# Kernel tuning notes

Hardware: AMD Instinct MI355X
Metric: run time of the kernel (lower is better)

The kernel has to match this reference:

```python
import jax, jax.numpy as jnp
import numpy as np

T, HID, H, KV, D = 2048, 2048, 16, 8, 128
EPS = 1e-6
THETA = 10000.0


def setup_inputs() -> dict:
    key = jax.random.key(0)
    ks = jax.random.split(key, 4)
    return {
        "positions": jnp.arange(T, dtype=jnp.int32),
        "hidden_states": jax.random.normal(ks[0], (T, HID), dtype=jnp.float32),
        "layernorm_weight": jnp.ones((HID,), dtype=jnp.float32),
        "qkv_weight": jax.random.normal(ks[1], ((H + 2 * KV) * D, HID), dtype=jnp.float32) * 0.02,
        "q_norm_weight": jnp.ones((D,), dtype=jnp.float32),
        "k_norm_weight": jnp.ones((D,), dtype=jnp.float32),
        "o_weight": jax.random.normal(ks[2], (HID, H * D), dtype=jnp.float32) * 0.02,
    }


def _rms(x, w, eps=EPS):
    var = jnp.mean(jnp.square(x), axis=-1, keepdims=True)
    return x * jax.lax.rsqrt(var + eps) * w


def _rope(x, pos):
    # NeoX-style rotary over full head_dim. x: [T, nH, D]
    inv_freq = 1.0 / (THETA ** (jnp.arange(0, D, 2, dtype=jnp.float32) / D))
    ang = pos.astype(jnp.float32)[:, None] * inv_freq  # [T, D/2]
    cos, sin = jnp.cos(ang)[:, None, :], jnp.sin(ang)[:, None, :]
    x1, x2 = x[..., : D // 2], x[..., D // 2 :]
    return jnp.concatenate([x1 * cos - x2 * sin, x2 * cos + x1 * sin], axis=-1)


def reference(positions, hidden_states, layernorm_weight, qkv_weight,
              q_norm_weight, k_norm_weight, o_weight):
    # Fused RMSNorm + QKV projection
    normed = _rms(hidden_states, layernorm_weight)                 # [T, HID]
    qkv = normed @ qkv_weight.T                                    # [T, (H+2KV)*D]
    q, k, v = jnp.split(qkv, [H * D, (H + KV) * D], axis=-1)
    q = _rms(q.reshape(T, H, D), q_norm_weight)                    # per-head q norm
    k = _rms(k.reshape(T, KV, D), k_norm_weight)                   # per-head k norm
    v = v.reshape(T, KV, D)
    # RoPE
    q = _rope(q, positions)
    k = _rope(k, positions)
    # GQA causal attention
    scale = D ** -0.5
    kr = jnp.repeat(k, H // KV, axis=1)                            # [T, H, D]
    vr = jnp.repeat(v, H // KV, axis=1)
    scores = jnp.einsum("qhd,khd->hqk", q, kr) * scale             # [H, T, T]
    mask = jnp.tril(jnp.ones((T, T), dtype=bool))
    scores = jnp.where(mask[None], scores, jnp.finfo(scores.dtype).min)
    attn = jax.nn.softmax(scores, axis=-1)
    out = jnp.einsum("hqk,khd->qhd", attn, vr).reshape(T, H * D)
    return out @ o_weight.T                                        # [T, HID]
```

## Files before the change

kernel.cpp:

```cpp
#include <hip/hip_runtime.h>
#include <cstdint>
#include <cstddef>

typedef __bf16 bf16;
typedef __attribute__((ext_vector_type(8))) __bf16 bf16x8;
typedef __attribute__((ext_vector_type(4))) __bf16 bf16x4v;
typedef __attribute__((ext_vector_type(4))) float f32x4;
typedef __attribute__((ext_vector_type(4))) short short4v;

#define T_N   2048
#define HID_N 2048
#define NH    16
#define NKV   8
#define HD    128

#define MFMA(a, b, c) __builtin_amdgcn_mfma_f32_16x16x32_bf16((a), (b), (c), 0, 0, 0)

__device__ __forceinline__ f32x4 MFMA16(short4v a, short4v b, f32x4 c) {
#if __has_builtin(__builtin_amdgcn_mfma_f32_16x16x16bf16_1k)
    return __builtin_amdgcn_mfma_f32_16x16x16bf16_1k(a, b, c, 0, 0, 0);
#else
    asm volatile("v_mfma_f32_16x16x16_bf16 %0, %1, %2, %0\n\ts_nop 7\n\ts_nop 7"
                 : "+v"(c) : "v"(a), "v"(b));
    return c;
#endif
}

__device__ __forceinline__ void gl_lds16(const void* g, void* l) {
    __builtin_amdgcn_global_load_lds(
        (const __attribute__((address_space(1))) unsigned int*)g,
        (__attribute__((address_space(3))) unsigned int*)l,
        16, 0, 0);
}

__device__ __forceinline__ uint32_t pk2(float a, float b) {
    union { bf16 h; unsigned short u; } ca, cb;
    ca.h = (bf16)a; cb.h = (bf16)b;
    return ((uint32_t)cb.u << 16) | ca.u;
}

__global__ __launch_bounds__(256) void k_f2b(const float* __restrict__ in,
                                             bf16* __restrict__ out, int n) {
    int i = (blockIdx.x * 256 + threadIdx.x) * 8;
    if (i >= n) return;
    const float4* p = (const float4*)(in + i);
    float4 a = p[0], b = p[1];
    bf16x8 v;
    v[0] = (bf16)a.x; v[1] = (bf16)a.y; v[2] = (bf16)a.z; v[3] = (bf16)a.w;
    v[4] = (bf16)b.x; v[5] = (bf16)b.y; v[6] = (bf16)b.z; v[7] = (bf16)b.w;
    *(bf16x8*)(out + i) = v;
}

__global__ __launch_bounds__(256) void k_rmsnorm(const float* __restrict__ x,
                                                 const float* __restrict__ w,
                                                 bf16* __restrict__ out) {
    int row = blockIdx.x, tid = threadIdx.x;
    const float* xr = x + (size_t)row * HID_N;
    float4 a = ((const float4*)xr)[tid * 2];
    float4 b = ((const float4*)xr)[tid * 2 + 1];
    float ss = a.x*a.x + a.y*a.y + a.z*a.z + a.w*a.w
             + b.x*b.x + b.y*b.y + b.z*b.z + b.w*b.w;
    #pragma unroll
    for (int m = 32; m; m >>= 1) ss += __shfl_xor(ss, m);
    __shared__ float red[4];
    if ((tid & 63) == 0) red[tid >> 6] = ss;
    __syncthreads();
    float tot = red[0] + red[1] + red[2] + red[3];
    float rs = rsqrtf(tot * (1.0f / HID_N) + 1e-6f);
    const float4* wr = (const float4*)(w + tid * 8);
    float4 wa = wr[0], wb = wr[1];
    bf16x8 v;
    v[0] = (bf16)(a.x * rs * wa.x); v[1] = (bf16)(a.y * rs * wa.y);
    v[2] = (bf16)(a.z * rs * wa.z); v[3] = (bf16)(a.w * rs * wa.w);
    v[4] = (bf16)(b.x * rs * wb.x); v[5] = (bf16)(b.y * rs * wb.y);
    v[6] = (bf16)(b.z * rs * wb.z); v[7] = (bf16)(b.w * rs * wb.w);
    *(bf16x8*)(out + (size_t)row * HID_N + tid * 8) = v;
}

__global__ __launch_bounds__(256, 2) void k_gemm_bt(const bf16* __restrict__ A,
                                                    const bf16* __restrict__ B,
                                                    float* __restrict__ C,
                                                    int M, int N, int K) {
    __shared__ __attribute__((aligned(16))) bf16 As[128 * 64];
    __shared__ __attribute__((aligned(16))) bf16 Bs[128 * 64];
    const int tid = threadIdx.x;
    const int lane = tid & 63, wid = tid >> 6;
    const int wm = wid >> 1, wn = wid & 1;
    const int r = lane & 15, g = lane >> 4;
    const size_t bm = (size_t)blockIdx.y * 128, bn = (size_t)blockIdx.x * 128;

    f32x4 acc[4][4] = {};

    const int srow = tid >> 3;
    const int schk = tid & 7;

    for (int k0 = 0; k0 < K; k0 += 64) {
        __syncthreads();
        #pragma unroll
        for (int c = 0; c < 4; c++) {
            int row = c * 32 + srow;
            int ka = (schk ^ (row & 7)) << 3;
            gl_lds16(A + (bm + row) * (size_t)K + k0 + ka,
                     (char*)As + c * 4096 + tid * 16);
            gl_lds16(B + (bn + row) * (size_t)K + k0 + ka,
                     (char*)Bs + c * 4096 + tid * 16);
        }
        __syncthreads();
        #pragma unroll
        for (int kk = 0; kk < 2; kk++) {
            bf16x8 af[4], bfr[4];
            #pragma unroll
            for (int m = 0; m < 4; m++) {
                int row = wm * 64 + m * 16 + r;
                af[m] = *(const bf16x8*)(As + row * 64 + (((kk * 4 + g) ^ (row & 7)) << 3));
            }
            #pragma unroll
            for (int n = 0; n < 4; n++) {
                int row = wn * 64 + n * 16 + r;
                bfr[n] = *(const bf16x8*)(Bs + row * 64 + (((kk * 4 + g) ^ (row & 7)) << 3));
            }
            #pragma unroll
            for (int m = 0; m < 4; m++)
                #pragma unroll
                for (int n = 0; n < 4; n++)
                    acc[m][n] = MFMA(af[m], bfr[n], acc[m][n]);
        }
    }
    #pragma unroll
    for (int m = 0; m < 4; m++)
        #pragma unroll
        for (int n = 0; n < 4; n++)
            #pragma unroll
            for (int j = 0; j < 4; j++) {
                size_t row = bm + wm * 64 + m * 16 + g * 4 + j;
                size_t col = bn + wn * 64 + n * 16 + r;
                C[row * (size_t)N + col] = acc[m][n][j];
            }
}

__global__ __launch_bounds__(128) void k_normrope(const float* __restrict__ qkv,
                                                  const float* __restrict__ qw,
                                                  const float* __restrict__ kw,
                                                  const int* __restrict__ pos,
                                                  bf16* __restrict__ q,
                                                  bf16* __restrict__ k,
                                                  bf16* __restrict__ v) {
    int t = blockIdx.x, hs = blockIdx.y, d = threadIdx.x;
    const float* base = qkv + (size_t)t * 4096;
    if (hs >= 24) {
        int hv = hs - 24;
        v[((size_t)t * NKV + hv) * HD + d] = (bf16)base[3072 + hv * 128 + d];
        return;
    }
    bool isq = hs < 16;
    int h = isq ? hs : hs - 16;
    float x = isq ? base[h * 128 + d] : base[2048 + h * 128 + d];
    float ss = x * x;
    #pragma unroll
    for (int m = 32; m; m >>= 1) ss += __shfl_xor(ss, m);
    __shared__ float red[2];
    if ((d & 63) == 0) red[d >> 6] = ss;
    __syncthreads();
    float rs = rsqrtf((red[0] + red[1]) * (1.0f / HD) + 1e-6f);
    float nx = x * rs * (isq ? qw[d] : kw[d]);
    __shared__ float sh[128];
    sh[d] = nx;
    __syncthreads();
    float other = sh[d ^ 64];
    int j = d & 63;
    float ang = (float)pos[t] * __powf(10000.f, -(float)j * (1.f / 64.f));
    float s, c;
    __sincosf(ang, &s, &c);
    float o = (d < 64) ? (nx * c - other * s) : (nx * c + other * s);
    bf16* dst = isq ? (q + ((size_t)t * NH + h) * HD + d)
                    : (k + ((size_t)t * NKV + h) * HD + d);
    *dst = (bf16)o;
}

__global__ __launch_bounds__(256, 2) void k_flash(const bf16* __restrict__ Q,
                                                  const bf16* __restrict__ K,
                                                  const bf16* __restrict__ V,
                                                  bf16* __restrict__ O) {
    __shared__ __attribute__((aligned(16))) bf16 Ks2[2][64 * 128];
    __shared__ __attribute__((aligned(16))) bf16 Vt2[2][128 * 64];

    const int tid = threadIdx.x, lane = tid & 63, w = tid >> 6;
    const int r = lane & 15, g = lane >> 4;
    const int h = blockIdx.x, by = blockIdx.y;
    const int qt = (by < 16) ? (2 * by) : (63 - 2 * by);
    const int q0 = qt * 64;
    const int gh = h >> 1;
    const int q0w = q0 + w * 16;

    const int rowk = tid >> 4, posc = tid & 15;
    const int vd = tid & 127, vhalf = tid >> 7;

    bf16x8 qf[4];
    #pragma unroll
    for (int ks = 0; ks < 4; ks++)
        qf[ks] = *(const bf16x8*)(Q + ((size_t)(q0w + r) * NH + h) * HD + ks * 32 + g * 8);

    f32x4 acc[8] = {};
    float m_run = -1e30f, l_run = 0.f;
    const float scale = 0.08838834764831845f;
    const int nt = qt + 1;

    {
        #pragma unroll
        for (int c = 0; c < 4; c++) {
            int row = c * 16 + rowk;
            int srcc = posc ^ (row & 7);
            gl_lds16(K + ((size_t)row * NKV + gh) * HD + srcc * 8,
                     (char*)&Ks2[0][0] + c * 4096 + tid * 16);
        }
        bf16x8 vr[4];
        #pragma unroll
        for (int it = 0; it < 4; it++) {
            int kb = vhalf + it * 2;
            const bf16* src = V + ((size_t)(kb * 8) * NKV + gh) * HD + vd;
            #pragma unroll
            for (int i = 0; i < 8; i++) vr[it][i] = src[(size_t)i * (NKV * HD)];
        }
        #pragma unroll
        for (int it = 0; it < 4; it++) {
            int kb = vhalf + it * 2;
            *(bf16x8*)(&Vt2[0][0] + vd * 64 + ((kb ^ (vd & 7)) * 8)) = vr[it];
        }
        __syncthreads();
    }

    for (int t = 0; t < nt; ++t) {
        const int b = t & 1;
        const int kv0 = t * 64;
        const bool pf = (t + 1 < nt);
        bf16x8 vr[4];
        if (pf) {
            const int kv1 = kv0 + 64;
            #pragma unroll
            for (int c = 0; c < 4; c++) {
                int row = c * 16 + rowk;
                int srcc = posc ^ (row & 7);
                gl_lds16(K + ((size_t)(kv1 + row) * NKV + gh) * HD + srcc * 8,
                         (char*)&Ks2[0][0] + (b ^ 1) * 16384 + c * 4096 + tid * 16);
            }
            #pragma unroll
            for (int it = 0; it < 4; it++) {
                int kb = vhalf + it * 2;
                const bf16* src = V + ((size_t)(kv1 + kb * 8) * NKV + gh) * HD + vd;
                #pragma unroll
                for (int i = 0; i < 8; i++) vr[it][i] = src[(size_t)i * (NKV * HD)];
            }
        }
        {
            const bf16* Kb = &Ks2[b][0];
            const char* Vb = (const char*)&Vt2[b][0];
            float sc[4][4];
            __builtin_amdgcn_s_setprio(1);
            #pragma unroll
            for (int t4 = 0; t4 < 4; t4++) {
                f32x4 S = {};
                #pragma unroll
                for (int ks = 0; ks < 4; ks++) {
                    int row = t4 * 16 + r;
                    bf16x8 kf = *(const bf16x8*)(Kb + row * 128 + (((4 * ks + g) ^ (row & 7)) * 8));
                    S = MFMA(kf, qf[ks], S);
                }
                #pragma unroll
                for (int j = 0; j < 4; j++) {
                    int kg = kv0 + t4 * 16 + 4 * g + j;
                    sc[t4][j] = (kg <= q0w + r) ? S[j] * scale : -1e30f;
                }
            }
            __builtin_amdgcn_s_setprio(0);
            float mx = sc[0][0];
            #pragma unroll
            for (int t4 = 0; t4 < 4; t4++)
                #pragma unroll
                for (int j = 0; j < 4; j++) mx = fmaxf(mx, sc[t4][j]);
            mx = fmaxf(mx, __shfl_xor(mx, 16));
            mx = fmaxf(mx, __shfl_xor(mx, 32));
            float mn = fmaxf(m_run, mx);
            float alpha = __expf(m_run - mn);
            m_run = mn;
            float rsum = 0.f;
            #pragma unroll
            for (int t4 = 0; t4 < 4; t4++)
                #pragma unroll
                for (int j = 0; j < 4; j++) {
                    sc[t4][j] = __expf(sc[t4][j] - mn);
                    rsum += sc[t4][j];
                }
            rsum += __shfl_xor(rsum, 16);
            rsum += __shfl_xor(rsum, 32);
            l_run = l_run * alpha + rsum;
            #pragma unroll
            for (int f = 0; f < 8; f++)
                #pragma unroll
                for (int j = 0; j < 4; j++) acc[f][j] *= alpha;
            union PB { uint32_t u[2]; short4v s; };
            PB pbu[4];
            #pragma unroll
            for (int t4 = 0; t4 < 4; t4++) {
                pbu[t4].u[0] = pk2(sc[t4][0], sc[t4][1]);
                pbu[t4].u[1] = pk2(sc[t4][2], sc[t4][3]);
            }
            __builtin_amdgcn_s_setprio(1);
            #pragma unroll
            for (int f = 0; f < 8; f++) {
                #pragma unroll
                for (int t4 = 0; t4 < 4; t4++) {
                    short4v vf = *(const short4v*)(Vb + f * 2048 + r * 128 +
                                  (((2 * t4 + (g >> 1)) ^ (r & 7)) * 16) + (g & 1) * 8);
                    acc[f] = MFMA16(vf, pbu[t4].s, acc[f]);
                }
            }
            __builtin_amdgcn_s_setprio(0);
        }
        if (pf) {
            #pragma unroll
            for (int it = 0; it < 4; it++) {
                int kb = vhalf + it * 2;
                *(bf16x8*)(&Vt2[0][0] + (b ^ 1) * 8192 + vd * 64 + ((kb ^ (vd & 7)) * 8)) = vr[it];
            }
        }
        __syncthreads();
    }
    float inv_l = 1.0f / l_run;
    #pragma unroll
    for (int f = 0; f < 8; f++) {
        bf16x4v ov;
        #pragma unroll
        for (int j = 0; j < 4; j++) ov[j] = (bf16)(acc[f][j] * inv_l);
        *(bf16x4v*)(O + ((size_t)(q0w + r) * NH + h) * HD + f * 16 + 4 * g) = ov;
    }
}

extern "C" void kernel_launch(void* const* d_in, const int* in_sizes, int n_in,
                              void* d_out, int out_size, void* d_ws, size_t ws_size,
                              hipStream_t stream) {
    const int*   pos  = (const int*)d_in[0];
    const float* hid  = (const float*)d_in[1];
    const float* lw   = (const float*)d_in[2];
    const float* qkvw = (const float*)d_in[3];
    const float* qnw  = (const float*)d_in[4];
    const float* knw  = (const float*)d_in[5];
    const float* ow   = (const float*)d_in[6];
    float* out = (float*)d_out;

    char* ws = (char*)d_ws;
    bf16*  qkvw_b = (bf16*)(ws);
    bf16*  ow_b   = (bf16*)(ws + (16u << 20));
    bf16*  normed = (bf16*)(ws + (24u << 20));
    float* qkvf   = (float*)(ws + (32u << 20));
    bf16*  qb     = (bf16*)(ws + (64u << 20));
    bf16*  kb     = (bf16*)(ws + (72u << 20));
    bf16*  vb     = (bf16*)(ws + (76u << 20));
    bf16*  ao     = normed;

    k_f2b<<<4096, 256, 0, stream>>>(qkvw, qkvw_b, 4096 * 2048);
    k_f2b<<<2048, 256, 0, stream>>>(ow, ow_b, 2048 * 2048);
    k_rmsnorm<<<T_N, 256, 0, stream>>>(hid, lw, normed);
    k_gemm_bt<<<dim3(32, 16), 256, 0, stream>>>(normed, qkvw_b, qkvf, 2048, 4096, 2048);
    k_normrope<<<dim3(T_N, 32), 128, 0, stream>>>(qkvf, qnw, knw, pos, qb, kb, vb);
    k_flash<<<dim3(NH, 32), 256, 0, stream>>>(qb, kb, vb, ao);
    k_gemm_bt<<<dim3(16, 16), 256, 0, stream>>>(ao, ow_b, out, 2048, 2048, 2048);
}
```

Before: 196.8 us.

## Split flash attention over KV chunks with separate combine kernel

Each query tile's causal KV range is cut into chunks of up to 8 KV tiles, so the grid grows from 512 to 1280 blocks. Each block writes a partial output plus running max and sum, and a new combine kernel merges them with log-sum-exp weights. The V tile is now single-buffered with an extra barrier, and occupancy is raised to 3 blocks per SM. This is meant to balance the uneven causal workload and fill the GPU better. The cost is an extra kernel launch, more global traffic for the partials, and extra synchronisation in the inner loop.

```diff
diff --git a/kernel.cpp b/kernel.cpp
--- a/kernel.cpp
+++ b/kernel.cpp
@@ -177,17 +177,24 @@
     *dst = (bf16)o;
 }
 
-__global__ __launch_bounds__(256, 2) void k_flash(const bf16* __restrict__ Q,
+__global__ __launch_bounds__(256, 3) void k_flash(const bf16* __restrict__ Q,
                                                   const bf16* __restrict__ K,
                                                   const bf16* __restrict__ V,
-                                                  bf16* __restrict__ O) {
+                                                  bf16* __restrict__ On,
+                                                  float* __restrict__ ml) {
     __shared__ __attribute__((aligned(16))) bf16 Ks2[2][64 * 128];
-    __shared__ __attribute__((aligned(16))) bf16 Vt2[2][128 * 64];
+    __shared__ __attribute__((aligned(16))) bf16 Vt[128 * 64];
 
     const int tid = threadIdx.x, lane = tid & 63, w = tid >> 6;
     const int r = lane & 15, g = lane >> 4;
-    const int h = blockIdx.x, by = blockIdx.y;
-    const int qt = (by < 16) ? (2 * by) : (63 - 2 * by);
+    const int h = blockIdx.x, y = blockIdx.y;
+    int ci, qt;
+    if (y < 32)      { ci = 0; qt = y; }
+    else if (y < 56) { ci = 1; qt = y - 24; }
+    else if (y < 72) { ci = 2; qt = y - 40; }
+    else             { ci = 3; qt = y - 48; }
+    const int c0 = ci * 8;
+    const int ntl = min(qt + 1 - c0, 8);
     const int q0 = qt * 64;
     const int gh = h >> 1;
     const int q0w = q0 + w * 16;
@@ -203,36 +210,36 @@
     f32x4 acc[8] = {};
     float m_run = -1e30f, l_run = 0.f;
     const float scale = 0.08838834764831845f;
-    const int nt = qt + 1;
 
     {
+        const int kv0 = c0 * 64;
         #pragma unroll
         for (int c = 0; c < 4; c++) {
             int row = c * 16 + rowk;
             int srcc = posc ^ (row & 7);
-            gl_lds16(K + ((size_t)row * NKV + gh) * HD + srcc * 8,
+            gl_lds16(K + ((size_t)(kv0 + row) * NKV + gh) * HD + srcc * 8,
                      (char*)&Ks2[0][0] + c * 4096 + tid * 16);
         }
         bf16x8 vr[4];
         #pragma unroll
         for (int it = 0; it < 4; it++) {
             int kb = vhalf + it * 2;
-            const bf16* src = V + ((size_t)(kb * 8) * NKV + gh) * HD + vd;
+            const bf16* src = V + ((size_t)(kv0 + kb * 8) * NKV + gh) * HD + vd;
             #pragma unroll
             for (int i = 0; i < 8; i++) vr[it][i] = src[(size_t)i * (NKV * HD)];
         }
         #pragma unroll
         for (int it = 0; it < 4; it++) {
             int kb = vhalf + it * 2;
-            *(bf16x8*)(&Vt2[0][0] + vd * 64 + ((kb ^ (vd & 7)) * 8)) = vr[it];
+            *(bf16x8*)(&Vt[0] + vd * 64 + ((kb ^ (vd & 7)) * 8)) = vr[it];
         }
         __syncthreads();
     }
 
-    for (int t = 0; t < nt; ++t) {
+    for (int t = 0; t < ntl; ++t) {
         const int b = t & 1;
-        const int kv0 = t * 64;
-        const bool pf = (t + 1 < nt);
+        const int kv0 = (c0 + t) * 64;
+        const bool pf = (t + 1 < ntl);
         bf16x8 vr[4];
         if (pf) {
             const int kv1 = kv0 + 64;
@@ -251,9 +258,9 @@
                 for (int i = 0; i < 8; i++) vr[it][i] = src[(size_t)i * (NKV * HD)];
             }
         }
-        {
+        if (kv0 <= q0w + 15) {
             const bf16* Kb = &Ks2[b][0];
-            const char* Vb = (const char*)&Vt2[b][0];
+            const char* Vb = (const char*)&Vt[0];
             float sc[4][4];
             __builtin_amdgcn_s_setprio(1);
             #pragma unroll
@@ -317,21 +324,71 @@
             __builtin_amdgcn_s_setprio(0);
         }
         if (pf) {
+            __syncthreads();
             #pragma unroll
             for (int it = 0; it < 4; it++) {
                 int kb = vhalf + it * 2;
-                *(bf16x8*)(&Vt2[0][0] + (b ^ 1) * 8192 + vd * 64 + ((kb ^ (vd & 7)) * 8)) = vr[it];
-            }
-        }
-        __syncthreads();
-    }
+                *(bf16x8*)(&Vt[0] + vd * 64 + ((kb ^ (vd & 7)) * 8)) = vr[it];
+            }
+            __syncthreads();
+        }
+    }
+    const int lr = w * 16 + r;
     float inv_l = 1.0f / l_run;
+    bf16* Ob = On + ((size_t)(h * 80 + y)) * 8192 + lr * 128;
     #pragma unroll
     for (int f = 0; f < 8; f++) {
         bf16x4v ov;
         #pragma unroll
         for (int j = 0; j < 4; j++) ov[j] = (bf16)(acc[f][j] * inv_l);
-        *(bf16x4v*)(O + ((size_t)(q0w + r) * NH + h) * HD + f * 16 + 4 * g) = ov;
+        *(bf16x4v*)(Ob + f * 16 + 4 * g) = ov;
+    }
+    if (g == 0) {
+        float* mlp = ml + ((size_t)(h * 80 + y)) * 128;
+        mlp[lr] = m_run;
+        mlp[64 + lr] = l_run;
+    }
+}
+
+__global__ __launch_bounds__(256) void k_comb(const bf16* __restrict__ On,
+                                              const float* __restrict__ ml,
+                                              bf16* __restrict__ ao) {
+    const int h = blockIdx.x, qt = blockIdx.y;
+    const int lr = threadIdx.x & 63, db = threadIdx.x >> 6;
+    const int nc = 1 + (qt >= 8) + (qt >= 16) + (qt >= 24);
+    const int ys[4] = {qt, qt + 24, qt + 40, qt + 48};
+    float mi[4], li[4], wi[4];
+    float mstar = -1e30f;
+    for (int i = 0; i < 4; i++) {
+        if (i < nc) {
+            const float* p = ml + ((size_t)(h * 80 + ys[i])) * 128;
+            mi[i] = p[lr]; li[i] = p[64 + lr];
+            mstar = fmaxf(mstar, mi[i]);
+        }
+    }
+    float wsum = 0.f;
+    for (int i = 0; i < 4; i++) {
+        if (i < nc) { wi[i] = li[i] * __expf(mi[i] - mstar); wsum += wi[i]; }
+        else wi[i] = 0.f;
+    }
+    float inv = 1.f / wsum;
+    for (int i = 0; i < 4; i++) wi[i] *= inv;
+    const int q = qt * 64 + lr;
+    #pragma unroll
+    for (int dd = 0; dd < 4; dd++) {
+        int d0 = db * 32 + dd * 8;
+        float o[8] = {};
+        for (int i = 0; i < 4; i++) {
+            if (i < nc) {
+                bf16x8 v = *(const bf16x8*)(On + ((size_t)(h * 80 + ys[i])) * 8192 + lr * 128 + d0);
+                #pragma unroll
+                for (int j = 0; j < 8; j++) o[j] += wi[i] * (float)v[j];
+            }
+        }
+        bf16x8 ov;
+        #pragma unroll
+        for (int j = 0; j < 8; j++) ov[j] = (bf16)o[j];
+        *(bf16x8*)(ao + ((size_t)q * NH + h) * HD + d0) = ov;
     }
 }
 
@@ -356,12 +413,15 @@
     bf16*  kb     = (bf16*)(ws + (72u << 20));
     bf16*  vb     = (bf16*)(ws + (76u << 20));
     bf16*  ao     = normed;
+    bf16*  On     = (bf16*)(ws + (32u << 20));
+    float* ml     = (float*)(ws + (54u << 20));
 
     k_f2b<<<4096, 256, 0, stream>>>(qkvw, qkvw_b, 4096 * 2048);
     k_f2b<<<2048, 256, 0, stream>>>(ow, ow_b, 2048 * 2048);
     k_rmsnorm<<<T_N, 256, 0, stream>>>(hid, lw, normed);
     k_gemm_bt<<<dim3(32, 16), 256, 0, stream>>>(normed, qkvw_b, qkvf, 2048, 4096, 2048);
     k_normrope<<<dim3(T_N, 32), 128, 0, stream>>>(qkvf, qnw, knw, pos, qb, kb, vb);
-    k_flash<<<dim3(NH, 32), 256, 0, stream>>>(qb, kb, vb, ao);
+    k_flash<<<dim3(NH, 80), 256, 0, stream>>>(qb, kb, vb, On, ml);
+    k_comb<<<dim3(NH, 32), 256, 0, stream>>>(On, ml, ao);
     k_gemm_bt<<<dim3(16, 16), 256, 0, stream>>>(ao, ow_b, out, 2048, 2048, 2048);
 }
```

Measured after the change: 185.7 us. -5.6%, faster.
